# Kernel tuning notes

Measured on AMD Instinct MI355X. Metric: run time of the kernel, lower is better.

The kernel has to match this reference:

```python
import jax, jax.numpy as jnp
import numpy as np

N_NODES = 62      # config.note_num (SEED EEG electrodes)
BATCH   = 1024    # graphs per batch
IN_CH   = 5
HID     = 64
OUT_CH  = 3
K_HOPS  = 2       # config.K


def setup_inputs() -> dict:
    key = jax.random.key(0)
    ks = jax.random.split(key, 8)
    total = BATCH * N_NODES
    x = jax.random.normal(ks[0], (total, IN_CH), dtype=jnp.float32)
    # fully-connected per-graph edge_index in row-major order (incl. self-loops),
    # matching edge_weight.reshape(-1).repeat(batch_size) in the torch code
    src = jnp.repeat(jnp.arange(N_NODES, dtype=jnp.int32), N_NODES)
    dst = jnp.tile(jnp.arange(N_NODES, dtype=jnp.int32), N_NODES)
    offs = (jnp.arange(BATCH, dtype=jnp.int32) * N_NODES)[:, None]
    edge_index = jnp.stack([
        (src[None, :] + offs).reshape(-1),
        (dst[None, :] + offs).reshape(-1),
    ])  # [2, BATCH*3844]
    batch = jnp.repeat(jnp.arange(BATCH, dtype=jnp.int32), N_NODES)
    n_tril = N_NODES * (N_NODES + 1) // 2  # 1953
    edge_weight_param = jax.random.normal(ks[1], (n_tril,), dtype=jnp.float32)
    w1 = jax.random.normal(ks[2], (HID, IN_CH), dtype=jnp.float32) * (1.0 / np.sqrt(IN_CH))
    b1 = jnp.zeros((HID,), dtype=jnp.float32)
    w2 = jax.random.normal(ks[3], (HID, HID), dtype=jnp.float32) * (1.0 / np.sqrt(HID))
    b2 = jnp.zeros((HID,), dtype=jnp.float32)
    wfc = jax.random.normal(ks[4], (OUT_CH, HID), dtype=jnp.float32) * (1.0 / np.sqrt(HID))
    bfc = jnp.zeros((OUT_CH,), dtype=jnp.float32)
    return dict(x=x, edge_index=edge_index, batch=batch,
                edge_weight_param=edge_weight_param,
                w1=w1, b1=b1, w2=w2, b2=b2, wfc=wfc, bfc=bfc)


def _gcn_norm(edge_index, edge_weight, num_nodes):
    # Graph already contains every self-loop, so add_remaining_self_loops only
    # reorders edges; normalization math is identical on the original edge set.
    row, col = edge_index[0], edge_index[1]
    deg = jax.ops.segment_sum(jnp.abs(edge_weight), row, num_segments=num_nodes)
    deg_inv_sqrt = jnp.where(deg > 0, jax.lax.rsqrt(deg), 0.0)
    return deg_inv_sqrt[row] * edge_weight * deg_inv_sqrt[col]


def _rsgconv(x, src, dst, norm, w, b):
    n = x.shape[0]
    for _ in range(K_HOPS):  # K propagation hops (gather-scale-scatter)
        x = jax.ops.segment_sum(norm[:, None] * x[src], dst, num_segments=n)
    return x @ w.T + b


def reference(x, edge_index, batch, edge_weight_param, w1, b1, w2, b2, wfc, bfc):
    num_nodes = x.shape[0]
    # rebuild symmetric dense 62x62 edge-weight matrix from learnable tril vector
    xs, ys = jnp.tril_indices(N_NODES)
    W = jnp.zeros((N_NODES, N_NODES), dtype=x.dtype).at[xs, ys].set(edge_weight_param)
    W = W + W.T - jnp.diag(jnp.diag(W))
    edge_weight = jnp.tile(W.reshape(-1), BATCH)  # [BATCH*3844]
    norm = _gcn_norm(edge_index, edge_weight, num_nodes)
    src, dst = edge_index[0], edge_index[1]
    h = jax.nn.relu(_rsgconv(x, src, dst, norm, w1, b1))
    h = jax.nn.relu(_rsgconv(h, src, dst, norm, w2, b2))
    pooled = jax.ops.segment_sum(h, batch, num_segments=BATCH)  # global_add_pool
    # dropout is identity in eval mode
    return pooled @ wfc.T + bfc
```

## Files before the change

kernel.cpp:

```cpp
#include <hip/hip_runtime.h>

#define NN 62
#define NP 64
#define NBATCH 1024
#define IN_CH 5
#define HID 64
#define OUT_CH 3
#define NTRIL 1953
#define H1S 72
#define GS 17

typedef _Float16 f16;
typedef f16 half8 __attribute__((ext_vector_type(8)));
typedef float floatx4 __attribute__((ext_vector_type(4)));

__global__ __launch_bounds__(64) void setup_k(const float* __restrict__ p,
                                              const float* __restrict__ w2,
                                              f16* __restrict__ a2h,
                                              f16* __restrict__ a2l,
                                              f16* __restrict__ w2h,
                                              f16* __restrict__ w2l) {
    __shared__ float sA[NN * NP];
    __shared__ float sDinv[NN];
    const int lane = threadIdx.x;
    const int n = blockIdx.x;

    {
        float wv = w2[n * HID + lane];
        f16 wh = (f16)wv;
        w2h[n * NP + lane] = wh;
        w2l[n * NP + lane] = (f16)(wv - (float)wh);
    }

    for (int i = lane; i < NN * NP; i += 64) sA[i] = 0.f;
    __syncthreads();

    for (int i = lane; i < NTRIL; i += 64) {
        int r = (int)((sqrtf(8.f * (float)i + 1.f) - 1.f) * 0.5f);
        while (r * (r + 1) / 2 > i) --r;
        while ((r + 1) * (r + 2) / 2 <= i) ++r;
        int c = i - r * (r + 1) / 2;
        float v = p[i];
        sA[r * NP + c] = v;
        sA[c * NP + r] = v;
    }
    __syncthreads();

    if (lane < NN) {
        float s = 0.f;
        for (int j = 0; j < NN; ++j) s += fabsf(sA[lane * NP + j]);
        sDinv[lane] = (s > 0.f) ? (1.0f / sqrtf(s)) : 0.f;
    }
    __syncthreads();

    for (int i = lane; i < NN * NP; i += 64) {
        int r = i >> 6, c = i & 63;
        float dc = (c < NN) ? sDinv[c] : 0.f;
        sA[i] = sDinv[r] * sA[i] * dc;
    }
    __syncthreads();

    float acc = 0.f;
    if (n < NN)
        for (int k = 0; k < NN; ++k) acc += sA[n * NP + k] * sA[k * NP + lane];
    f16 ah = (f16)acc;
    a2h[n * NP + lane] = ah;
    a2l[n * NP + lane] = (f16)(acc - (float)ah);
}

__global__ __launch_bounds__(256, 4) void graph_net(
    const float* __restrict__ x,
    const f16* __restrict__ a2h, const f16* __restrict__ a2l,
    const f16* __restrict__ w2h, const f16* __restrict__ w2l,
    const float* __restrict__ w1, const float* __restrict__ b1,
    const float* __restrict__ b2,
    const float* __restrict__ wfc, const float* __restrict__ bfc,
    float* __restrict__ out) {
    __shared__ __align__(16) char smem[37120];
    f16* sUTh = (f16*)smem;
    f16* sUTl = (f16*)(smem + 9216);
    float* sG  = (float*)smem;
    f16* sH1h = (f16*)(smem + 18432);
    f16* sH1l = (f16*)(smem + 27648);
    float* sPool = (float*)(smem + 36864);

    const int t = threadIdx.x;
    const int lane = t & 63;
    const int w = __builtin_amdgcn_readfirstlane(t >> 6);
    const int g = blockIdx.x;
    const float* xg = x + (size_t)g * (NN * IN_CH);

    const int jn = lane & 15;
    const int qd = lane >> 4;
    const int jglob = 16 * w + jn;

    half8 aFh[4][2], aFl[4][2];
#pragma unroll
    for (int T = 0; T < 4; ++T)
#pragma unroll
        for (int ks = 0; ks < 2; ++ks) {
            aFh[T][ks] = *(const half8*)(a2h + (16 * T + jn) * NP + qd * 8 + 32 * ks);
            aFl[T][ks] = *(const half8*)(a2l + (16 * T + jn) * NP + qd * 8 + 32 * ks);
        }

    int xi[IN_CH];
    {
        const int L = (lane < NN) ? lane : (NN - 1);
        const int* xgi = (const int*)xg;
#pragma unroll
        for (int c = 0; c < IN_CH; ++c) xi[c] = xgi[L * IN_CH + c];
    }
    float w1r[IN_CH];
#pragma unroll
    for (int c = 0; c < IN_CH; ++c) w1r[c] = w1[lane * IN_CH + c];

#pragma unroll
    for (int ni = 0; ni < 16; ++ni) {
        const int n = 16 * w + ni;
        if (n < NN) {
            float u = 0.f;
#pragma unroll
            for (int c = 0; c < IN_CH; ++c)
                u += __int_as_float(__builtin_amdgcn_readlane(xi[c], n)) * w1r[c];
            f16 uh = (f16)u;
            sUTh[lane * H1S + n] = uh;
            sUTl[lane * H1S + n] = (f16)(u - (float)uh);
        }
    }
    if (t < 128) {
        const int n = 62 + (t >> 6);
        sUTh[(t & 63) * H1S + n] = (f16)0.f;
        sUTl[(t & 63) * H1S + n] = (f16)0.f;
    }
    __syncthreads();

    half8 bUh[2], bUl[2];
#pragma unroll
    for (int ks = 0; ks < 2; ++ks) {
        bUh[ks] = *(const half8*)(sUTh + jglob * H1S + qd * 8 + 32 * ks);
        bUl[ks] = *(const half8*)(sUTl + jglob * H1S + qd * 8 + 32 * ks);
    }
    floatx4 C1[4];
#pragma unroll
    for (int T = 0; T < 4; ++T) { C1[T][0]=0.f; C1[T][1]=0.f; C1[T][2]=0.f; C1[T][3]=0.f; }
#pragma unroll
    for (int T = 0; T < 4; ++T) {
#pragma unroll
        for (int ks = 0; ks < 2; ++ks) {
            C1[T] = __builtin_amdgcn_mfma_f32_16x16x32_f16(aFl[T][ks], bUh[ks], C1[T], 0, 0, 0);
            C1[T] = __builtin_amdgcn_mfma_f32_16x16x32_f16(aFh[T][ks], bUl[ks], C1[T], 0, 0, 0);
            C1[T] = __builtin_amdgcn_mfma_f32_16x16x32_f16(aFh[T][ks], bUh[ks], C1[T], 0, 0, 0);
        }
    }
    {
        const float b1r = b1[jglob];
#pragma unroll
        for (int T = 0; T < 4; ++T)
#pragma unroll
            for (int r = 0; r < 4; ++r) {
                const int n = 16 * T + qd * 4 + r;
                float v = fmaxf(C1[T][r] + b1r, 0.f);
                f16 vh = (f16)v;
                sH1h[n * H1S + jglob] = vh;
                sH1l[n * H1S + jglob] = (f16)(v - (float)vh);
            }
    }
    __syncthreads();

    half8 bWh[2], bWl[2];
#pragma unroll
    for (int ks = 0; ks < 2; ++ks) {
        bWh[ks] = *(const half8*)(w2h + jglob * NP + qd * 8 + 32 * ks);
        bWl[ks] = *(const half8*)(w2l + jglob * NP + qd * 8 + 32 * ks);
    }
    floatx4 Cg[4];
#pragma unroll
    for (int T = 0; T < 4; ++T) { Cg[T][0]=0.f; Cg[T][1]=0.f; Cg[T][2]=0.f; Cg[T][3]=0.f; }
#pragma unroll
    for (int T = 0; T < 4; ++T) {
#pragma unroll
        for (int ks = 0; ks < 2; ++ks) {
            const half8 aH = *(const half8*)(sH1h + (16 * T + jn) * H1S + qd * 8 + 32 * ks);
            const half8 aL = *(const half8*)(sH1l + (16 * T + jn) * H1S + qd * 8 + 32 * ks);
            Cg[T] = __builtin_amdgcn_mfma_f32_16x16x32_f16(aL, bWh[ks], Cg[T], 0, 0, 0);
            Cg[T] = __builtin_amdgcn_mfma_f32_16x16x32_f16(aH, bWl[ks], Cg[T], 0, 0, 0);
            Cg[T] = __builtin_amdgcn_mfma_f32_16x16x32_f16(aH, bWh[ks], Cg[T], 0, 0, 0);
        }
    }
    {
        float* gw = sG + w * (NP * GS);
#pragma unroll
        for (int T = 0; T < 4; ++T)
#pragma unroll
            for (int r = 0; r < 4; ++r)
                gw[(16 * T + qd * 4 + r) * GS + jn] = Cg[T][r];
    }
    __syncthreads();

    half8 bGh[2], bGl[2];
    {
        const float* gr = sG + w * (NP * GS);
#pragma unroll
        for (int ks = 0; ks < 2; ++ks)
#pragma unroll
            for (int i = 0; i < 8; ++i) {
                float v = gr[(qd * 8 + i + 32 * ks) * GS + jn];
                f16 vh = (f16)v;
                bGh[ks][i] = vh;
                bGl[ks][i] = (f16)(v - (float)vh);
            }
    }

    floatx4 C2[4];
#pragma unroll
    for (int T = 0; T < 4; ++T) { C2[T][0]=0.f; C2[T][1]=0.f; C2[T][2]=0.f; C2[T][3]=0.f; }
#pragma unroll
    for (int T = 0; T < 4; ++T) {
#pragma unroll
        for (int ks = 0; ks < 2; ++ks) {
            C2[T] = __builtin_amdgcn_mfma_f32_16x16x32_f16(aFl[T][ks], bGh[ks], C2[T], 0, 0, 0);
            C2[T] = __builtin_amdgcn_mfma_f32_16x16x32_f16(aFh[T][ks], bGl[ks], C2[T], 0, 0, 0);
            C2[T] = __builtin_amdgcn_mfma_f32_16x16x32_f16(aFh[T][ks], bGh[ks], C2[T], 0, 0, 0);
        }
    }

    {
        const float b2r = b2[jglob];
        float pool = 0.f;
#pragma unroll
        for (int T = 0; T < 4; ++T)
#pragma unroll
            for (int r = 0; r < 4; ++r) {
                const int n = 16 * T + qd * 4 + r;
                float v = fmaxf(C2[T][r] + b2r, 0.f);
                pool += (n < NN) ? v : 0.f;
            }
        pool += __shfl_xor(pool, 16);
        pool += __shfl_xor(pool, 32);
        if (lane < 16) sPool[jglob] = pool;
    }
    __syncthreads();

    if (t < OUT_CH) {
        float v = bfc[t];
        const float* wr = wfc + t * HID;
#pragma unroll
        for (int m = 0; m < HID; ++m) v += sPool[m] * wr[m];
        out[g * OUT_CH + t] = v;
    }
}

extern "C" void kernel_launch(void* const* d_in, const int* in_sizes, int n_in,
                              void* d_out, int out_size, void* d_ws, size_t ws_size,
                              hipStream_t stream) {
    const float* x   = (const float*)d_in[0];
    const float* ewp = (const float*)d_in[3];
    const float* w1  = (const float*)d_in[4];
    const float* b1  = (const float*)d_in[5];
    const float* w2  = (const float*)d_in[6];
    const float* b2  = (const float*)d_in[7];
    const float* wfc = (const float*)d_in[8];
    const float* bfc = (const float*)d_in[9];
    float* out = (float*)d_out;

    f16* a2h = (f16*)d_ws;
    f16* a2l = a2h + NP * NP;
    f16* w2h = a2l + NP * NP;
    f16* w2l = w2h + NP * NP;

    setup_k<<<NP, 64, 0, stream>>>(ewp, w2, a2h, a2l, w2h, w2l);
    graph_net<<<NBATCH, 256, 0, stream>>>(x, a2h, a2l, w2h, w2l,
                                          w1, b1, b2, wfc, bfc, out);
}
```

Before: 124.9 us.

## Fuse adjacency-squared setup into graph kernel and drop the separate setup launch

The separate setup kernel is removed. Each graph block now rebuilds the normalized 62x62 adjacency from the tril parameters in shared memory, squares it with split-f16 MFMA, and converts W2 to hi/lo f16 from global fp32. This removes a kernel launch and the dependency between the two kernels, at the cost of redundant per-block setup work and extra barriers. It also drops one barrier between the per-wave G write and read, and replaces the serial 3-thread FC with a wave-shuffle reduction.

Result: faster. 107.3 us (-14.1%).

```diff
diff --git a/kernel.cpp b/kernel.cpp
--- a/kernel.cpp
+++ b/kernel.cpp
@@ -9,79 +9,31 @@
 #define NTRIL 1953
 #define H1S 72
 #define GS 17
+#define SAS 68
 
 typedef _Float16 f16;
 typedef f16 half8 __attribute__((ext_vector_type(8)));
 typedef float floatx4 __attribute__((ext_vector_type(4)));
 
-__global__ __launch_bounds__(64) void setup_k(const float* __restrict__ p,
-                                              const float* __restrict__ w2,
-                                              f16* __restrict__ a2h,
-                                              f16* __restrict__ a2l,
-                                              f16* __restrict__ w2h,
-                                              f16* __restrict__ w2l) {
-    __shared__ float sA[NN * NP];
-    __shared__ float sDinv[NN];
-    const int lane = threadIdx.x;
-    const int n = blockIdx.x;
-
-    {
-        float wv = w2[n * HID + lane];
-        f16 wh = (f16)wv;
-        w2h[n * NP + lane] = wh;
-        w2l[n * NP + lane] = (f16)(wv - (float)wh);
-    }
-
-    for (int i = lane; i < NN * NP; i += 64) sA[i] = 0.f;
-    __syncthreads();
-
-    for (int i = lane; i < NTRIL; i += 64) {
-        int r = (int)((sqrtf(8.f * (float)i + 1.f) - 1.f) * 0.5f);
-        while (r * (r + 1) / 2 > i) --r;
-        while ((r + 1) * (r + 2) / 2 <= i) ++r;
-        int c = i - r * (r + 1) / 2;
-        float v = p[i];
-        sA[r * NP + c] = v;
-        sA[c * NP + r] = v;
-    }
-    __syncthreads();
-
-    if (lane < NN) {
-        float s = 0.f;
-        for (int j = 0; j < NN; ++j) s += fabsf(sA[lane * NP + j]);
-        sDinv[lane] = (s > 0.f) ? (1.0f / sqrtf(s)) : 0.f;
-    }
-    __syncthreads();
-
-    for (int i = lane; i < NN * NP; i += 64) {
-        int r = i >> 6, c = i & 63;
-        float dc = (c < NN) ? sDinv[c] : 0.f;
-        sA[i] = sDinv[r] * sA[i] * dc;
-    }
-    __syncthreads();
-
-    float acc = 0.f;
-    if (n < NN)
-        for (int k = 0; k < NN; ++k) acc += sA[n * NP + k] * sA[k * NP + lane];
-    f16 ah = (f16)acc;
-    a2h[n * NP + lane] = ah;
-    a2l[n * NP + lane] = (f16)(acc - (float)ah);
-}
-
 __global__ __launch_bounds__(256, 4) void graph_net(
     const float* __restrict__ x,
-    const f16* __restrict__ a2h, const f16* __restrict__ a2l,
-    const f16* __restrict__ w2h, const f16* __restrict__ w2l,
+    const float* __restrict__ ewp,
     const float* __restrict__ w1, const float* __restrict__ b1,
-    const float* __restrict__ b2,
+    const float* __restrict__ w2, const float* __restrict__ b2,
     const float* __restrict__ wfc, const float* __restrict__ bfc,
     float* __restrict__ out) {
     __shared__ __align__(16) char smem[37120];
+    f16* sAh = (f16*)smem;
+    f16* sAl = (f16*)(smem + 9216);
     f16* sUTh = (f16*)smem;
     f16* sUTl = (f16*)(smem + 9216);
-    float* sG  = (float*)smem;
+    float* sG = (float*)smem;
+    float* sA = (float*)(smem + 18432);
+    f16* sA2h = (f16*)(smem + 18432);
+    f16* sA2l = (f16*)(smem + 27648);
     f16* sH1h = (f16*)(smem + 18432);
     f16* sH1l = (f16*)(smem + 27648);
+    float* sDinv = (float*)(smem + 36864);
     float* sPool = (float*)(smem + 36864);
 
     const int t = threadIdx.x;
@@ -94,15 +46,6 @@
     const int qd = lane >> 4;
     const int jglob = 16 * w + jn;
 
-    half8 aFh[4][2], aFl[4][2];
-#pragma unroll
-    for (int T = 0; T < 4; ++T)
-#pragma unroll
-        for (int ks = 0; ks < 2; ++ks) {
-            aFh[T][ks] = *(const half8*)(a2h + (16 * T + jn) * NP + qd * 8 + 32 * ks);
-            aFl[T][ks] = *(const half8*)(a2l + (16 * T + jn) * NP + qd * 8 + 32 * ks);
-        }
-
     int xi[IN_CH];
     {
         const int L = (lane < NN) ? lane : (NN - 1);
@@ -113,6 +56,84 @@
     float w1r[IN_CH];
 #pragma unroll
     for (int c = 0; c < IN_CH; ++c) w1r[c] = w1[lane * IN_CH + c];
+
+#pragma unroll
+    for (int k = 0; k < 8; ++k) {
+        int i = t + 256 * k;
+        if (i < NTRIL) {
+            int r = (int)((sqrtf(8.f * (float)i + 1.f) - 1.f) * 0.5f);
+            while (r * (r + 1) / 2 > i) --r;
+            while ((r + 1) * (r + 2) / 2 <= i) ++r;
+            int c = i - r * (r + 1) / 2;
+            float v = ewp[i];
+            sA[r * SAS + c] = v;
+            sA[c * SAS + r] = v;
+        }
+    }
+    __syncthreads();
+
+    if (t < NN) {
+        float s0 = 0.f, s1 = 0.f;
+        for (int j = 0; j < NN; j += 2) {
+            s0 += fabsf(sA[t * SAS + j]);
+            s1 += fabsf(sA[t * SAS + j + 1]);
+        }
+        float s = s0 + s1;
+        sDinv[t] = (s > 0.f) ? (1.0f / sqrtf(s)) : 0.f;
+    }
+    __syncthreads();
+
+#pragma unroll
+    for (int k = 0; k < 16; ++k) {
+        int idx = t + 256 * k;
+        int r = idx >> 6, c = idx & 63;
+        float v = (r < NN && c < NN) ? sDinv[r] * sA[r * SAS + c] * sDinv[c] : 0.f;
+        f16 vh = (f16)v;
+        sAh[r * H1S + c] = vh;
+        sAl[r * H1S + c] = (f16)(v - (float)vh);
+    }
+    __syncthreads();
+
+    half8 bSh[2], bSl[2];
+#pragma unroll
+    for (int ks = 0; ks < 2; ++ks) {
+        bSh[ks] = *(const half8*)(sAh + jglob * H1S + qd * 8 + 32 * ks);
+        bSl[ks] = *(const half8*)(sAl + jglob * H1S + qd * 8 + 32 * ks);
+    }
+    floatx4 D2[4];
+#pragma unroll
+    for (int T = 0; T < 4; ++T) { D2[T][0]=0.f; D2[T][1]=0.f; D2[T][2]=0.f; D2[T][3]=0.f; }
+#pragma unroll
+    for (int T = 0; T < 4; ++T) {
+#pragma unroll
+        for (int ks = 0; ks < 2; ++ks) {
+            const half8 ah = *(const half8*)(sAh + (16 * T + jn) * H1S + qd * 8 + 32 * ks);
+            const half8 al = *(const half8*)(sAl + (16 * T + jn) * H1S + qd * 8 + 32 * ks);
+            D2[T] = __builtin_amdgcn_mfma_f32_16x16x32_f16(al, bSh[ks], D2[T], 0, 0, 0);
+            D2[T] = __builtin_amdgcn_mfma_f32_16x16x32_f16(ah, bSl[ks], D2[T], 0, 0, 0);
+            D2[T] = __builtin_amdgcn_mfma_f32_16x16x32_f16(ah, bSh[ks], D2[T], 0, 0, 0);
+        }
+    }
+#pragma unroll
+    for (int T = 0; T < 4; ++T)
+#pragma unroll
+        for (int r = 0; r < 4; ++r) {
+            const int n = 16 * T + qd * 4 + r;
+            float v = D2[T][r];
+            f16 vh = (f16)v;
+            sA2h[n * H1S + jglob] = vh;
+            sA2l[n * H1S + jglob] = (f16)(v - (float)vh);
+        }
+    __syncthreads();
+
+    half8 aFh[4][2], aFl[4][2];
+#pragma unroll
+    for (int T = 0; T < 4; ++T)
+#pragma unroll
+        for (int ks = 0; ks < 2; ++ks) {
+            aFh[T][ks] = *(const half8*)(sA2h + (16 * T + jn) * H1S + qd * 8 + 32 * ks);
+            aFl[T][ks] = *(const half8*)(sA2l + (16 * T + jn) * H1S + qd * 8 + 32 * ks);
+        }
 
 #pragma unroll
     for (int ni = 0; ni < 16; ++ni) {
@@ -165,14 +186,26 @@
                 sH1l[n * H1S + jglob] = (f16)(v - (float)vh);
             }
     }
+    floatx4 w2lo[2], w2hi[2];
+#pragma unroll
+    for (int ks = 0; ks < 2; ++ks) {
+        w2lo[ks] = *(const floatx4*)(w2 + jglob * HID + qd * 8 + 32 * ks);
+        w2hi[ks] = *(const floatx4*)(w2 + jglob * HID + qd * 8 + 32 * ks + 4);
+    }
     __syncthreads();
 
     half8 bWh[2], bWl[2];
 #pragma unroll
-    for (int ks = 0; ks < 2; ++ks) {
-        bWh[ks] = *(const half8*)(w2h + jglob * NP + qd * 8 + 32 * ks);
-        bWl[ks] = *(const half8*)(w2l + jglob * NP + qd * 8 + 32 * ks);
-    }
+    for (int ks = 0; ks < 2; ++ks)
+#pragma unroll
+        for (int i = 0; i < 4; ++i) {
+            f16 h0 = (f16)w2lo[ks][i];
+            bWh[ks][i] = h0;
+            bWl[ks][i] = (f16)(w2lo[ks][i] - (float)h0);
+            f16 h1 = (f16)w2hi[ks][i];
+            bWh[ks][4 + i] = h1;
+            bWl[ks][4 + i] = (f16)(w2hi[ks][i] - (float)h1);
+        }
     floatx4 Cg[4];
 #pragma unroll
     for (int T = 0; T < 4; ++T) { Cg[T][0]=0.f; Cg[T][1]=0.f; Cg[T][2]=0.f; Cg[T][3]=0.f; }
@@ -195,7 +228,6 @@
             for (int r = 0; r < 4; ++r)
                 gw[(16 * T + qd * 4 + r) * GS + jn] = Cg[T][r];
     }
-    __syncthreads();
 
     half8 bGh[2], bGl[2];
     {
@@ -241,12 +273,19 @@
     }
     __syncthreads();
 
-    if (t < OUT_CH) {
-        float v = bfc[t];
-        const float* wr = wfc + t * HID;
-#pragma unroll
-        for (int m = 0; m < HID; ++m) v += sPool[m] * wr[m];
-        out[g * OUT_CH + t] = v;
+    if (t < HID) {
+        const float pv = sPool[t];
+#pragma unroll
+        for (int o = 0; o < OUT_CH; ++o) {
+            float vv = pv * wfc[o * HID + t];
+            vv += __shfl_xor(vv, 1);
+            vv += __shfl_xor(vv, 2);
+            vv += __shfl_xor(vv, 4);
+            vv += __shfl_xor(vv, 8);
+            vv += __shfl_xor(vv, 16);
+            vv += __shfl_xor(vv, 32);
+            if (t == 0) out[g * OUT_CH + o] = vv + bfc[o];
+        }
     }
 }
 
@@ -262,13 +301,7 @@
     const float* wfc = (const float*)d_in[8];
     const float* bfc = (const float*)d_in[9];
     float* out = (float*)d_out;
-
-    f16* a2h = (f16*)d_ws;
-    f16* a2l = a2h + NP * NP;
-    f16* w2h = a2l + NP * NP;
-    f16* w2l = w2h + NP * NP;
-
-    setup_k<<<NP, 64, 0, stream>>>(ewp, w2, a2h, a2l, w2h, w2l);
-    graph_net<<<NBATCH, 256, 0, stream>>>(x, a2h, a2l, w2h, w2l,
-                                          w1, b1, b2, wfc, bfc, out);
+    (void)d_ws; (void)ws_size;
+
+    graph_net<<<NBATCH, 256, 0, stream>>>(x, ewp, w1, b1, w2, b2, wfc, bfc, out);
 }
```
